# Optimization experiments

Hardware: AMD Instinct MI355X
Metric: run time of the kernel (lower is better)

Reference implementation:

```python
import jax, jax.numpy as jnp
import numpy as np

RADIUS = 0.1
NSAMPLE = 32


def _ball_query(new_xyz, xyz, radius, nsample):
    # new_xyz: (B, S, 3), xyz: (B, N, 3) -> idx (B, S, nsample) int32
    N = xyz.shape[1]
    d2 = jnp.sum((new_xyz[:, :, None, :] - xyz[:, None, :, :]) ** 2, axis=-1)  # (B,S,N)
    mask = d2 < radius * radius
    cand = jnp.where(mask, jnp.arange(N, dtype=jnp.int32)[None, None, :], N)
    cand = jnp.sort(cand, axis=-1)[:, :, :nsample]  # first nsample in-ball indices
    first = cand[:, :, :1]
    first = jnp.where(first == N, 0, first)  # empty ball -> index 0 (CUDA semantics)
    return jnp.where(cand == N, first, cand).astype(jnp.int32)


def _group(features, idx):
    # features: (B, C, N), idx: (B, S, K) -> (B, C, S, K)
    return jax.vmap(lambda f, i: f[:, i])(features, idx)


def setup_inputs() -> dict:
    key = jax.random.key(0)
    k1, k2, k3, k4 = jax.random.split(key, 4)
    B, N, S, C = 4, 16384, 2048, 64
    xyz = jax.random.uniform(k1, (B, N, 3), dtype=jnp.float32)
    new_xyz = jax.random.uniform(k2, (B, S, 3), dtype=jnp.float32)
    features = jax.random.normal(k3, (B, C, N), dtype=jnp.float32)
    fps_idx = jax.random.randint(k4, (B, S), 0, N, dtype=jnp.int32)
    return {"xyz": xyz, "new_xyz": new_xyz, "features": features, "fps_idx": fps_idx}


def reference(xyz, new_xyz, features, fps_idx):
    idx = _ball_query(new_xyz, xyz, RADIUS, NSAMPLE)          # (B,S,nsample)
    idx = jnp.concatenate([fps_idx[:, :, None], idx], axis=2)  # (B,S,nsample+1)
    xyz_t = jnp.transpose(xyz, (0, 2, 1))                      # (B,3,N)
    raw_grouped_xyz = _group(xyz_t, idx)                       # (B,3,S,K)
    grouped_xyz = raw_grouped_xyz - jnp.transpose(new_xyz, (0, 2, 1))[..., None]
    grouped_features = _group(features, idx)                   # (B,C,S,K)
    return jnp.concatenate([raw_grouped_xyz, grouped_xyz, grouped_features], axis=1)
```

## Files before the change

kernel.cpp:

```cpp
#include <hip/hip_runtime.h>

#define BB 4
#define NN 16384
#define SS 2048
#define CC 64
#define NS 32
#define KK 33
#define OC 70
#define SCH 4
#define GT 512
#define NC 10
#define NCELL 1000
#define HCAP 224
#define RPAD 0.100001f

__device__ __forceinline__ float sq_nofma(float v) {
  float r = v * v;
  asm volatile("" : "+v"(r));
  return r;
}

__device__ __forceinline__ int cell1(float x) {
  int c = (int)(x * 10.0f);
  return c < 0 ? 0 : (c > 9 ? 9 : c);
}
__device__ __forceinline__ int cell3(float x, float y, float z) {
  return (cell1(z) * NC + cell1(y)) * NC + cell1(x);
}

__device__ __forceinline__ void ball_query_wave(
    const float* __restrict__ xb, float qx, float qy, float qz, int lane,
    int* out) {
  const float R2 = 0.01f;
  int cnt = 0;
  int firstIdx = 0;
  for (int base = 0; base < NN; base += 256) {
    float px[4], py[4], pz[4];
#pragma unroll
    for (int j = 0; j < 4; ++j) {
      int n = base + j * 64 + lane;
      const float* p = xb + n * 3;
      px[j] = p[0]; py[j] = p[1]; pz[j] = p[2];
    }
#pragma unroll
    for (int j = 0; j < 4; ++j) {
      float dx = px[j] - qx, dy = py[j] - qy, dz = pz[j] - qz;
      float d2 = sq_nofma(dx) + sq_nofma(dy);
      asm volatile("" : "+v"(d2));
      d2 = d2 + sq_nofma(dz);
      bool m = d2 < R2;
      unsigned long long bal = __ballot(m);
      if (cnt == 0 && bal) firstIdx = base + j * 64 + __builtin_ctzll(bal);
      int pos = cnt + (int)__popcll(bal & ((1ull << lane) - 1ull));
      if (m && pos < NS) out[pos] = base + j * 64 + lane;
      cnt += (int)__popcll(bal);
    }
    if (cnt >= NS) break;
  }
  if (cnt < NS) {
    int pad = (cnt == 0) ? 0 : firstIdx;
    if (lane >= cnt && lane < NS) out[lane] = pad;
  }
}

__global__ __launch_bounds__(256) void qg_tr_hist2(
    const float* __restrict__ xyz, const float* __restrict__ feat,
    float* __restrict__ featT, int* __restrict__ partial) {
  __shared__ float tile[32 * 260];
  __shared__ int h[1024];
  const int bid = (int)blockIdx.x;
  const int tid = (int)threadIdx.x;
  const int b = bid >> 7;
  const int rest = bid & 127;
  const int n0 = (rest >> 1) << 8;
  const int cc = rest & 1;
  const int c0 = cc << 5;
  const int wv = tid >> 6, lane = tid & 63;

  if (cc == 0) {
#pragma unroll
    for (int c = tid; c < 1024; c += 256) h[c] = 0;
    __syncthreads();
    const float* p = xyz + ((size_t)b * NN + n0 + tid) * 3;
    atomicAdd(&h[cell3(p[0], p[1], p[2])], 1);
  }

  const float* fb = feat + ((size_t)b * CC + c0) * NN + n0;
#pragma unroll
  for (int rr = 0; rr < 8; ++rr) {
    int c = rr * 4 + wv;
    float4 v = *(const float4*)(fb + (size_t)c * NN + 4 * lane);
    *(float4*)&tile[c * 260 + 4 * lane] = v;
  }
  __syncthreads();
  const int c4 = lane & 7, m = lane >> 3;
  float4* oT = (float4*)(featT + ((size_t)b * NN + n0) * CC);
#pragma unroll
  for (int it = 0; it < 8; ++it) {
    int n = it * 32 + wv * 8 + m;
    float4 v;
    v.x = tile[(4 * c4 + 0) * 260 + n];
    v.y = tile[(4 * c4 + 1) * 260 + n];
    v.z = tile[(4 * c4 + 2) * 260 + n];
    v.w = tile[(4 * c4 + 3) * 260 + n];
    oT[(size_t)n * (CC / 4) + (c0 >> 2) + c4] = v;
  }

  if (cc == 0) {
    const int j = rest >> 1;
    int* pr = partial + (((size_t)b * 128 + j) << 10);
#pragma unroll
    for (int c = tid; c < 1024; c += 256) pr[c] = h[c];
  }
}

__global__ __launch_bounds__(256) void qg_scan2(
    const int* __restrict__ partial, int* __restrict__ off,
    int* __restrict__ woff) {
  __shared__ int sc[256];
  const int b = (int)blockIdx.x;
  const int tid = (int)threadIdx.x;
  int l0 = 0, l1 = 0, l2 = 0, l3 = 0;
  for (int j = 0; j < 64; j += 4) {
#pragma unroll
    for (int jj = 0; jj < 4; ++jj) {
      const int4 v = ((const int4*)(partial + (((size_t)b * 128 + j + jj) << 10)))[tid];
      l0 += v.x; l1 += v.y; l2 += v.z; l3 += v.w;
    }
  }
  int base = tid * 4;
  int s1 = l0, s2 = l0 + l1, s3 = l0 + l1 + l2, tot = s3 + l3;
  sc[tid] = tot;
  __syncthreads();
  for (int d = 1; d < 256; d <<= 1) {
    int v = (tid >= d) ? sc[tid - d] : 0;
    __syncthreads();
    sc[tid] += v;
    __syncthreads();
  }
  int ex = sc[tid] - tot;
  int* offb = off + b * (NCELL + 1);
  int* woffb = woff + b * NCELL;
  if (base + 0 < NCELL) { offb[base + 0] = ex;      woffb[base + 0] = ex; }
  if (base + 1 < NCELL) { offb[base + 1] = ex + s1; woffb[base + 1] = ex + s1; }
  if (base + 2 < NCELL) { offb[base + 2] = ex + s2; woffb[base + 2] = ex + s2; }
  if (base + 3 < NCELL) { offb[base + 3] = ex + s3; woffb[base + 3] = ex + s3; }
  if (tid == 0) offb[NCELL] = NN;
}

__global__ __launch_bounds__(256) void qg_scatter(
    const float* __restrict__ xyz, int* __restrict__ woff,
    float4* __restrict__ pts) {
  int i = (int)(blockIdx.x * 256u + threadIdx.x);
  int b = i >> 14, n = i & (NN - 1);
  const float* p = xyz + ((size_t)b * NN + n) * 3;
  float x = p[0], y = p[1], z = p[2];
  int cell = cell3(x, y, z);
  int pos = atomicAdd(&woff[b * NCELL + cell], 1);
  pts[(b << 14) + pos] = make_float4(x, y, z, __int_as_float(n));
}

__global__ __launch_bounds__(256) void qg_query(
    const float* __restrict__ xyz, const float* __restrict__ nxyz,
    const float4* __restrict__ pts, const int* __restrict__ off,
    int* __restrict__ wsidx) {
  __shared__ int hitbuf[4][HCAP];
  __shared__ int hcnt_s[4];
  const int tid = (int)threadIdx.x;
  const int wv = tid >> 6, lane = tid & 63;
  const int q = (int)blockIdx.x * 4 + wv;
  const int b = q >> 11;
  const float R2 = 0.01f;
  float qx = nxyz[q * 3 + 0];
  float qy = nxyz[q * 3 + 1];
  float qz = nxyz[q * 3 + 2];
  int* hb = hitbuf[wv];
  int* outp = wsidx + (size_t)q * NS;
  if (lane == 0) hcnt_s[wv] = 0;
  asm volatile("s_waitcnt lgkmcnt(0)" ::: "memory");

  int lox = max(0, (int)floorf((qx - RPAD) * 10.f));
  int hix = min(9, (int)floorf((qx + RPAD) * 10.f));
  int loy = max(0, (int)floorf((qy - RPAD) * 10.f));
  int hiy = min(9, (int)floorf((qy + RPAD) * 10.f));
  int loz = max(0, (int)floorf((qz - RPAD) * 10.f));
  int hiz = min(9, (int)floorf((qz + RPAD) * 10.f));

  const int* offb = off + b * (NCELL + 1);
  int start_l = 0, end_l = 0;
  {
    int cz = loz + lane / 3, cy = loy + lane % 3;
    if (lane < 9 && cz <= hiz && cy <= hiy) {
      int row = (cz * NC + cy) * NC;
      start_l = offb[row + lox];
      end_l = offb[row + hix + 1];
    }
  }
  const float4* pb = pts + ((size_t)b << 14);
  for (int sp = 0; sp < 9; ++sp) {
    int start = __shfl(start_l, sp, 64);
    int end = __shfl(end_l, sp, 64);
    for (int p0 = start; p0 < end; p0 += 64) {
      int ii = p0 + lane;
      bool valid = ii < end;
      float4 v = pb[valid ? ii : (end - 1)];
      float dx = v.x - qx, dy = v.y - qy, dz = v.z - qz;
      float d2 = sq_nofma(dx) + sq_nofma(dy);
      asm volatile("" : "+v"(d2));
      d2 = d2 + sq_nofma(dz);
      if (valid && d2 < R2) {
        int pos = atomicAdd(&hcnt_s[wv], 1);
        if (pos < HCAP) hb[pos] = __float_as_int(v.w);
      }
    }
  }
  asm volatile("s_waitcnt lgkmcnt(0)" ::: "memory");
  const int M = hcnt_s[wv];
  if (M > HCAP) {
    ball_query_wave(xyz + (size_t)b * NN * 3, qx, qy, qz, lane, outp);
    return;
  }
  int minv = 0x7fffffff;
  for (int i = lane; i < M; i += 64) {
    int hh = hb[i];
    minv = min(minv, hh);
    int rank = 0;
    for (int j = 0; j < M; ++j) rank += (hb[j] < hh) ? 1 : 0;
    if (rank < NS) outp[rank] = hh;
  }
  if (M < NS) {
#pragma unroll
    for (int d = 1; d < 64; d <<= 1) minv = min(minv, __shfl_xor(minv, d, 64));
    int pad = (M == 0) ? 0 : minv;
    if (lane >= M && lane < NS) outp[lane] = pad;
  }
}

__global__ __launch_bounds__(GT) void qg_gather2(
    const float* __restrict__ xyz, const float* __restrict__ nxyz,
    const float* __restrict__ featT, const int* __restrict__ fps,
    const int* __restrict__ wsidx, float* __restrict__ out) {
  __shared__ float sf[CC][SCH * KK + 1];
  __shared__ int sidx[SCH * KK];
  const int tid = (int)threadIdx.x;
  const int blk = (int)blockIdx.x;
  const int b = blk >> 9;
  const int s0 = (blk & 511) * SCH;
  const size_t cstr = (size_t)SS * KK;

  if (tid < SCH * KK) {
    int s4 = tid / KK, k = tid - s4 * KK;
    int q = b * SS + s0 + s4;
    sidx[tid] = (k == 0) ? fps[q] : wsidx[(size_t)q * NS + (k - 1)];
  }
  __syncthreads();

  const float4* fT4 = (const float4*)(featT + (size_t)b * NN * CC);
  int e = tid & 15;
  for (int pp = tid >> 4; pp < SCH * KK; pp += GT / 16) {
    int n = sidx[pp];
    float4 v = fT4[(size_t)n * (CC / 4) + e];
    sf[4 * e + 0][pp] = v.x;
    sf[4 * e + 1][pp] = v.y;
    sf[4 * e + 2][pp] = v.z;
    sf[4 * e + 3][pp] = v.w;
  }

  if (tid < SCH * KK) {
    int s4 = tid / KK;
    int n = sidx[tid];
    const float* p = xyz + ((size_t)b * NN + n) * 3;
    float x = p[0], y = p[1], z = p[2];
    int q = b * SS + s0 + s4;
    float cx = nxyz[q * 3 + 0], cy = nxyz[q * 3 + 1], cz = nxyz[q * 3 + 2];
    size_t obase = ((size_t)(b * OC) * SS + s0) * KK + tid;
    out[obase + 0 * cstr] = x;
    out[obase + 1 * cstr] = y;
    out[obase + 2 * cstr] = z;
    out[obase + 3 * cstr] = x - cx;
    out[obase + 4 * cstr] = y - cy;
    out[obase + 5 * cstr] = z - cz;
  }
  __syncthreads();

  size_t fbase = ((size_t)(b * OC + 6) * SS + s0) * KK;
  for (int idx = tid; idx < CC * SCH * KK; idx += GT) {
    int c = idx / (SCH * KK);
    int j = idx - c * (SCH * KK);
    out[fbase + (size_t)c * cstr + j] = sf[c][j];
  }
}

__global__ __launch_bounds__(256) void qg_ballq(
    const float* __restrict__ xyz, const float* __restrict__ nxyz,
    int* __restrict__ wsidx) {
  int q = (int)((blockIdx.x * blockDim.x + threadIdx.x) >> 6);
  int lane = (int)(threadIdx.x & 63);
  int b = q / SS;
  const float* xb = xyz + (size_t)b * NN * 3;
  ball_query_wave(xb, nxyz[q * 3], nxyz[q * 3 + 1], nxyz[q * 3 + 2], lane,
                  wsidx + (size_t)q * NS);
}

__global__ __launch_bounds__(256) void qg_gather(
    const float* __restrict__ xyz, const float* __restrict__ nxyz,
    const float* __restrict__ feat, const int* __restrict__ fps,
    const int* __restrict__ wsidx, float* __restrict__ out) {
  unsigned t = blockIdx.x * 256u + threadIdx.x;
  const unsigned TOT = (unsigned)BB * OC * SS * KK;
  if (t >= TOT) return;
  unsigned k = t % KK;
  unsigned r = t / KK;
  unsigned s = r % SS;
  r /= SS;
  unsigned c = r % OC;
  unsigned b = r / OC;
  unsigned q = b * SS + s;
  int n = (k == 0) ? fps[q] : wsidx[(size_t)q * NS + (k - 1)];
  float v;
  if (c < 6) {
    unsigned cc = (c < 3) ? c : c - 3;
    v = xyz[((size_t)b * NN + (unsigned)n) * 3 + cc];
    if (c >= 3) v -= nxyz[q * 3 + cc];
  } else {
    v = feat[((size_t)b * CC + (c - 6)) * NN + (unsigned)n];
  }
  out[t] = v;
}

__global__ __launch_bounds__(256) void qg_fused(
    const float* __restrict__ xyz, const float* __restrict__ nxyz,
    const float* __restrict__ feat, const int* __restrict__ fps,
    float* __restrict__ out) {
  __shared__ int sidx[4][KK];
  int wv = (int)(threadIdx.x >> 6), lane = (int)(threadIdx.x & 63);
  int q = (int)blockIdx.x * 4 + wv;
  int b = q / SS, s = q % SS;
  const float* xb = xyz + (size_t)b * NN * 3;
  ball_query_wave(xb, nxyz[q * 3], nxyz[q * 3 + 1], nxyz[q * 3 + 2], lane,
                  &sidx[wv][1]);
  if (lane == 0) sidx[wv][0] = fps[q];
  __syncthreads();
  for (int f = lane; f < OC * KK; f += 64) {
    int c = f / KK, k = f - c * KK;
    int n = sidx[wv][k];
    float v;
    if (c < 6) {
      int cc = (c < 3) ? c : c - 3;
      v = xb[n * 3 + cc];
      if (c >= 3) v -= nxyz[q * 3 + cc];
    } else {
      v = feat[((size_t)b * CC + (c - 6)) * NN + n];
    }
    out[((size_t)((size_t)b * OC + c) * SS + s) * KK + k] = v;
  }
}

extern "C" void kernel_launch(void* const* d_in, const int* in_sizes, int n_in,
                              void* d_out, int out_size, void* d_ws, size_t ws_size,
                              hipStream_t stream) {
  const float* xyz  = (const float*)d_in[0];
  const float* nxyz = (const float*)d_in[1];
  const float* feat = (const float*)d_in[2];
  const int*   fps  = (const int*)d_in[3];
  float* out = (float*)d_out;

  const size_t pts_b     = (size_t)BB * NN * sizeof(float4);
  const size_t off_b     = 16384;
  const size_t partial_b = (size_t)BB * 128 * 1024 * sizeof(int);
  const size_t woff_b    = 16384;
  const size_t idx_b     = (size_t)BB * SS * NS * sizeof(int);
  const size_t featT_b   = (size_t)BB * NN * CC * sizeof(float);
  const size_t grid_need = pts_b + off_b + partial_b + woff_b + idx_b + featT_b;

  if (ws_size >= grid_need) {
    char* w = (char*)d_ws;
    float4* pts     = (float4*)w;                    w += pts_b;
    int*    off     = (int*)w;                       w += off_b;
    int*    partial = (int*)w;                       w += partial_b;
    int*    woff    = (int*)w;                       w += woff_b;
    int*    wsidx   = (int*)w;                       w += idx_b;
    float*  featT   = (float*)w;
    qg_tr_hist2<<<512, 256, 0, stream>>>(xyz, feat, featT, partial);
    qg_scan2<<<BB, 256, 0, stream>>>(partial, off, woff);
    qg_scatter<<<(BB * NN) / 256, 256, 0, stream>>>(xyz, woff, pts);
    qg_query<<<(BB * SS) / 4, 256, 0, stream>>>(xyz, nxyz, pts, off, wsidx);
    qg_gather2<<<BB * (SS / SCH), GT, 0, stream>>>(xyz, nxyz, featT, fps,
                                                   wsidx, out);
  } else if (ws_size >= idx_b + featT_b) {
    int* wsidx = (int*)d_ws;
    float* featT = (float*)((char*)d_ws + idx_b);
    qg_ballq<<<(BB * SS) / 4, 256, 0, stream>>>(xyz, nxyz, wsidx);
    unsigned tot = (unsigned)BB * OC * SS * KK;
    qg_gather<<<(tot + 255u) / 256u, 256, 0, stream>>>(xyz, nxyz, feat, fps,
                                                       wsidx, out);
  } else if (ws_size >= idx_b) {
    int* wsidx = (int*)d_ws;
    qg_ballq<<<(BB * SS) / 4, 256, 0, stream>>>(xyz, nxyz, wsidx);
    unsigned tot = (unsigned)BB * OC * SS * KK;
    qg_gather<<<(tot + 255u) / 256u, 256, 0, stream>>>(xyz, nxyz, feat, fps,
                                                       wsidx, out);
  } else {
    qg_fused<<<(BB * SS) / 4, 256, 0, stream>>>(xyz, nxyz, feat, fps, out);
  }
}
```

Baseline: 59.65 us.

## Replace histogram/scan/scatter grid build with fixed-capacity cell buckets and fuse query into gather

Points are bucketed straight into fixed 64-slot cells with a global atomic counter, which removes the histogram, prefix-scan and scatter kernels. A per-batch overflow flag falls back to brute-force ball query when any cell overflows. The ball query now runs inside the gather kernel, writing indices to shared memory and dropping the global index buffer and one launch. The cost is global atomics during the build, a memset, and wasted lanes on sparsely filled cells.

```diff
diff --git a/kernel.cpp b/kernel.cpp
--- a/kernel.cpp
+++ b/kernel.cpp
@@ -11,6 +11,7 @@
 #define GT 512
 #define NC 10
 #define NCELL 1000
+#define CCAP 64
 #define HCAP 224
 #define RPAD 0.100001f
 
@@ -63,11 +64,11 @@
   }
 }
 
-__global__ __launch_bounds__(256) void qg_tr_hist2(
+__global__ __launch_bounds__(256) void qg_tr_build(
     const float* __restrict__ xyz, const float* __restrict__ feat,
-    float* __restrict__ featT, int* __restrict__ partial) {
+    float* __restrict__ featT, int* __restrict__ cnt, int* __restrict__ ovf,
+    float4* __restrict__ ptsc) {
   __shared__ float tile[32 * 260];
-  __shared__ int h[1024];
   const int bid = (int)blockIdx.x;
   const int tid = (int)threadIdx.x;
   const int b = bid >> 7;
@@ -78,11 +79,17 @@
   const int wv = tid >> 6, lane = tid & 63;
 
   if (cc == 0) {
-#pragma unroll
-    for (int c = tid; c < 1024; c += 256) h[c] = 0;
-    __syncthreads();
-    const float* p = xyz + ((size_t)b * NN + n0 + tid) * 3;
-    atomicAdd(&h[cell3(p[0], p[1], p[2])], 1);
+    const int n = n0 + tid;
+    const float* p = xyz + ((size_t)b * NN + n) * 3;
+    float x = p[0], y = p[1], z = p[2];
+    int cell = cell3(x, y, z);
+    int pos = atomicAdd(&cnt[(b << 10) + cell], 1);
+    if (pos < CCAP) {
+      ptsc[((((size_t)b << 10) + cell) << 6) + pos] =
+          make_float4(x, y, z, __int_as_float(n));
+    } else {
+      atomicOr(&ovf[b], 1);
+    }
   }
 
   const float* fb = feat + ((size_t)b * CC + c0) * NN + n0;
@@ -105,156 +112,92 @@
     v.w = tile[(4 * c4 + 3) * 260 + n];
     oT[(size_t)n * (CC / 4) + (c0 >> 2) + c4] = v;
   }
-
-  if (cc == 0) {
-    const int j = rest >> 1;
-    int* pr = partial + (((size_t)b * 128 + j) << 10);
-#pragma unroll
-    for (int c = tid; c < 1024; c += 256) pr[c] = h[c];
-  }
-}
-
-__global__ __launch_bounds__(256) void qg_scan2(
-    const int* __restrict__ partial, int* __restrict__ off,
-    int* __restrict__ woff) {
-  __shared__ int sc[256];
-  const int b = (int)blockIdx.x;
-  const int tid = (int)threadIdx.x;
-  int l0 = 0, l1 = 0, l2 = 0, l3 = 0;
-  for (int j = 0; j < 64; j += 4) {
-#pragma unroll
-    for (int jj = 0; jj < 4; ++jj) {
-      const int4 v = ((const int4*)(partial + (((size_t)b * 128 + j + jj) << 10)))[tid];
-      l0 += v.x; l1 += v.y; l2 += v.z; l3 += v.w;
-    }
-  }
-  int base = tid * 4;
-  int s1 = l0, s2 = l0 + l1, s3 = l0 + l1 + l2, tot = s3 + l3;
-  sc[tid] = tot;
-  __syncthreads();
-  for (int d = 1; d < 256; d <<= 1) {
-    int v = (tid >= d) ? sc[tid - d] : 0;
-    __syncthreads();
-    sc[tid] += v;
-    __syncthreads();
-  }
-  int ex = sc[tid] - tot;
-  int* offb = off + b * (NCELL + 1);
-  int* woffb = woff + b * NCELL;
-  if (base + 0 < NCELL) { offb[base + 0] = ex;      woffb[base + 0] = ex; }
-  if (base + 1 < NCELL) { offb[base + 1] = ex + s1; woffb[base + 1] = ex + s1; }
-  if (base + 2 < NCELL) { offb[base + 2] = ex + s2; woffb[base + 2] = ex + s2; }
-  if (base + 3 < NCELL) { offb[base + 3] = ex + s3; woffb[base + 3] = ex + s3; }
-  if (tid == 0) offb[NCELL] = NN;
-}
-
-__global__ __launch_bounds__(256) void qg_scatter(
-    const float* __restrict__ xyz, int* __restrict__ woff,
-    float4* __restrict__ pts) {
-  int i = (int)(blockIdx.x * 256u + threadIdx.x);
-  int b = i >> 14, n = i & (NN - 1);
-  const float* p = xyz + ((size_t)b * NN + n) * 3;
-  float x = p[0], y = p[1], z = p[2];
-  int cell = cell3(x, y, z);
-  int pos = atomicAdd(&woff[b * NCELL + cell], 1);
-  pts[(b << 14) + pos] = make_float4(x, y, z, __int_as_float(n));
-}
-
-__global__ __launch_bounds__(256) void qg_query(
+}
+
+__global__ __launch_bounds__(GT) void qg_main(
     const float* __restrict__ xyz, const float* __restrict__ nxyz,
-    const float4* __restrict__ pts, const int* __restrict__ off,
-    int* __restrict__ wsidx) {
-  __shared__ int hitbuf[4][HCAP];
-  __shared__ int hcnt_s[4];
-  const int tid = (int)threadIdx.x;
-  const int wv = tid >> 6, lane = tid & 63;
-  const int q = (int)blockIdx.x * 4 + wv;
-  const int b = q >> 11;
-  const float R2 = 0.01f;
-  float qx = nxyz[q * 3 + 0];
-  float qy = nxyz[q * 3 + 1];
-  float qz = nxyz[q * 3 + 2];
-  int* hb = hitbuf[wv];
-  int* outp = wsidx + (size_t)q * NS;
-  if (lane == 0) hcnt_s[wv] = 0;
-  asm volatile("s_waitcnt lgkmcnt(0)" ::: "memory");
-
-  int lox = max(0, (int)floorf((qx - RPAD) * 10.f));
-  int hix = min(9, (int)floorf((qx + RPAD) * 10.f));
-  int loy = max(0, (int)floorf((qy - RPAD) * 10.f));
-  int hiy = min(9, (int)floorf((qy + RPAD) * 10.f));
-  int loz = max(0, (int)floorf((qz - RPAD) * 10.f));
-  int hiz = min(9, (int)floorf((qz + RPAD) * 10.f));
-
-  const int* offb = off + b * (NCELL + 1);
-  int start_l = 0, end_l = 0;
-  {
-    int cz = loz + lane / 3, cy = loy + lane % 3;
-    if (lane < 9 && cz <= hiz && cy <= hiy) {
-      int row = (cz * NC + cy) * NC;
-      start_l = offb[row + lox];
-      end_l = offb[row + hix + 1];
-    }
-  }
-  const float4* pb = pts + ((size_t)b << 14);
-  for (int sp = 0; sp < 9; ++sp) {
-    int start = __shfl(start_l, sp, 64);
-    int end = __shfl(end_l, sp, 64);
-    for (int p0 = start; p0 < end; p0 += 64) {
-      int ii = p0 + lane;
-      bool valid = ii < end;
-      float4 v = pb[valid ? ii : (end - 1)];
-      float dx = v.x - qx, dy = v.y - qy, dz = v.z - qz;
-      float d2 = sq_nofma(dx) + sq_nofma(dy);
-      asm volatile("" : "+v"(d2));
-      d2 = d2 + sq_nofma(dz);
-      if (valid && d2 < R2) {
-        int pos = atomicAdd(&hcnt_s[wv], 1);
-        if (pos < HCAP) hb[pos] = __float_as_int(v.w);
-      }
-    }
-  }
-  asm volatile("s_waitcnt lgkmcnt(0)" ::: "memory");
-  const int M = hcnt_s[wv];
-  if (M > HCAP) {
-    ball_query_wave(xyz + (size_t)b * NN * 3, qx, qy, qz, lane, outp);
-    return;
-  }
-  int minv = 0x7fffffff;
-  for (int i = lane; i < M; i += 64) {
-    int hh = hb[i];
-    minv = min(minv, hh);
-    int rank = 0;
-    for (int j = 0; j < M; ++j) rank += (hb[j] < hh) ? 1 : 0;
-    if (rank < NS) outp[rank] = hh;
-  }
-  if (M < NS) {
-#pragma unroll
-    for (int d = 1; d < 64; d <<= 1) minv = min(minv, __shfl_xor(minv, d, 64));
-    int pad = (M == 0) ? 0 : minv;
-    if (lane >= M && lane < NS) outp[lane] = pad;
-  }
-}
-
-__global__ __launch_bounds__(GT) void qg_gather2(
-    const float* __restrict__ xyz, const float* __restrict__ nxyz,
-    const float* __restrict__ featT, const int* __restrict__ fps,
-    const int* __restrict__ wsidx, float* __restrict__ out) {
+    const float4* __restrict__ ptsc, const int* __restrict__ cnt,
+    const int* __restrict__ ovf, const float* __restrict__ featT,
+    const int* __restrict__ fps, float* __restrict__ out) {
   __shared__ float sf[CC][SCH * KK + 1];
   __shared__ int sidx[SCH * KK];
+  __shared__ int hitbuf[SCH][HCAP];
+  __shared__ int hcnt_s[SCH];
   const int tid = (int)threadIdx.x;
   const int blk = (int)blockIdx.x;
   const int b = blk >> 9;
   const int s0 = (blk & 511) * SCH;
+  const int wv = tid >> 6, lane = tid & 63;
+
+  if (wv < SCH) {
+    const int q = b * SS + s0 + wv;
+    const float R2 = 0.01f;
+    float qx = nxyz[q * 3 + 0];
+    float qy = nxyz[q * 3 + 1];
+    float qz = nxyz[q * 3 + 2];
+    int* hb = hitbuf[wv];
+    int* qout = &sidx[wv * KK];
+    if (lane == 0) hcnt_s[wv] = 0;
+    asm volatile("s_waitcnt lgkmcnt(0)" ::: "memory");
+
+    if (ovf[b]) {
+      ball_query_wave(xyz + (size_t)b * NN * 3, qx, qy, qz, lane, qout + 1);
+    } else {
+      int lox = max(0, (int)floorf((qx - RPAD) * 10.f));
+      int hix = min(9, (int)floorf((qx + RPAD) * 10.f));
+      int loy = max(0, (int)floorf((qy - RPAD) * 10.f));
+      int hiy = min(9, (int)floorf((qy + RPAD) * 10.f));
+      int loz = max(0, (int)floorf((qz - RPAD) * 10.f));
+      int hiz = min(9, (int)floorf((qz + RPAD) * 10.f));
+
+      const int* cntb = cnt + (b << 10);
+      const float4* pcb = ptsc + ((size_t)b << 16);
+      for (int cz = loz; cz <= hiz; ++cz) {
+        for (int cy = loy; cy <= hiy; ++cy) {
+          int rowb = (cz * NC + cy) * NC;
+          for (int cx = lox; cx <= hix; ++cx) {
+            int cell = rowb + cx;
+            int m = cntb[cell];
+            if (m == 0) continue;
+            float4 v = pcb[(cell << 6) + lane];
+            float dx = v.x - qx, dy = v.y - qy, dz = v.z - qz;
+            float d2 = sq_nofma(dx) + sq_nofma(dy);
+            asm volatile("" : "+v"(d2));
+            d2 = d2 + sq_nofma(dz);
+            if (lane < m && d2 < R2) {
+              int pos = atomicAdd(&hcnt_s[wv], 1);
+              if (pos < HCAP) hb[pos] = __float_as_int(v.w);
+            }
+          }
+        }
+      }
+      asm volatile("s_waitcnt lgkmcnt(0)" ::: "memory");
+      const int M = hcnt_s[wv];
+      if (M > HCAP) {
+        ball_query_wave(xyz + (size_t)b * NN * 3, qx, qy, qz, lane, qout + 1);
+      } else {
+        int minv = 0x7fffffff;
+        for (int i = lane; i < M; i += 64) {
+          int hh = hb[i];
+          minv = min(minv, hh);
+          int rank = 0;
+          for (int j = 0; j < M; ++j) rank += (hb[j] < hh) ? 1 : 0;
+          if (rank < NS) qout[1 + rank] = hh;
+        }
+        if (M < NS) {
+#pragma unroll
+          for (int d = 1; d < 64; d <<= 1)
+            minv = min(minv, __shfl_xor(minv, d, 64));
+          int pad = (M == 0) ? 0 : minv;
+          if (lane >= M && lane < NS) qout[1 + lane] = pad;
+        }
+      }
+    }
+    if (lane == 0) qout[0] = fps[q];
+  }
+  __syncthreads();
+
   const size_t cstr = (size_t)SS * KK;
-
-  if (tid < SCH * KK) {
-    int s4 = tid / KK, k = tid - s4 * KK;
-    int q = b * SS + s0 + s4;
-    sidx[tid] = (k == 0) ? fps[q] : wsidx[(size_t)q * NS + (k - 1)];
-  }
-  __syncthreads();
-
   const float4* fT4 = (const float4*)(featT + (size_t)b * NN * CC);
   int e = tid & 15;
   for (int pp = tid >> 4; pp < SCH * KK; pp += GT / 16) {
@@ -365,35 +308,23 @@
   const int*   fps  = (const int*)d_in[3];
   float* out = (float*)d_out;
 
-  const size_t pts_b     = (size_t)BB * NN * sizeof(float4);
-  const size_t off_b     = 16384;
-  const size_t partial_b = (size_t)BB * 128 * 1024 * sizeof(int);
-  const size_t woff_b    = 16384;
-  const size_t idx_b     = (size_t)BB * SS * NS * sizeof(int);
-  const size_t featT_b   = (size_t)BB * NN * CC * sizeof(float);
-  const size_t grid_need = pts_b + off_b + partial_b + woff_b + idx_b + featT_b;
+  const size_t ptsc_b  = (size_t)BB * 1024 * CCAP * sizeof(float4);
+  const size_t cnt_b   = 32768;
+  const size_t featT_b = (size_t)BB * NN * CC * sizeof(float);
+  const size_t grid_need = ptsc_b + cnt_b + featT_b;
+
+  const size_t idx_b = (size_t)BB * SS * NS * sizeof(int);
 
   if (ws_size >= grid_need) {
     char* w = (char*)d_ws;
-    float4* pts     = (float4*)w;                    w += pts_b;
-    int*    off     = (int*)w;                       w += off_b;
-    int*    partial = (int*)w;                       w += partial_b;
-    int*    woff    = (int*)w;                       w += woff_b;
-    int*    wsidx   = (int*)w;                       w += idx_b;
-    float*  featT   = (float*)w;
-    qg_tr_hist2<<<512, 256, 0, stream>>>(xyz, feat, featT, partial);
-    qg_scan2<<<BB, 256, 0, stream>>>(partial, off, woff);
-    qg_scatter<<<(BB * NN) / 256, 256, 0, stream>>>(xyz, woff, pts);
-    qg_query<<<(BB * SS) / 4, 256, 0, stream>>>(xyz, nxyz, pts, off, wsidx);
-    qg_gather2<<<BB * (SS / SCH), GT, 0, stream>>>(xyz, nxyz, featT, fps,
-                                                   wsidx, out);
-  } else if (ws_size >= idx_b + featT_b) {
-    int* wsidx = (int*)d_ws;
-    float* featT = (float*)((char*)d_ws + idx_b);
-    qg_ballq<<<(BB * SS) / 4, 256, 0, stream>>>(xyz, nxyz, wsidx);
-    unsigned tot = (unsigned)BB * OC * SS * KK;
-    qg_gather<<<(tot + 255u) / 256u, 256, 0, stream>>>(xyz, nxyz, feat, fps,
-                                                       wsidx, out);
+    float4* ptsc  = (float4*)w;                      w += ptsc_b;
+    int*    cnt   = (int*)w;                         w += cnt_b;
+    float*  featT = (float*)w;
+    int*    ovf   = cnt + BB * 1024;
+    hipMemsetAsync(cnt, 0, cnt_b, stream);
+    qg_tr_build<<<512, 256, 0, stream>>>(xyz, feat, featT, cnt, ovf, ptsc);
+    qg_main<<<BB * (SS / SCH), GT, 0, stream>>>(xyz, nxyz, ptsc, cnt, ovf,
+                                                featT, fps, out);
   } else if (ws_size >= idx_b) {
     int* wsidx = (int*)d_ws;
     qg_ballq<<<(BB * SS) / 4, 256, 0, stream>>>(xyz, nxyz, wsidx);
```

After: 67.58 us. +13.3%, slower.
